# Performance work log

Hardware: AMD Instinct MI355X
Metric: run time of the kernel (lower is better)

## Reference

```python
import jax, jax.numpy as jnp
import numpy as np

WD = 8        # window_dim
E = 32        # embedding_dim
D = E * WD * WD   # attention_dim = 2048
NH = 8        # num_heads (SwinTransformer default)
B, H, W = 16, 64, 64
NW = (H // WD) * (W // WD)  # 64 windows
FF = 4 * D


def _partition(x):
    # 'b (vp vw) (hp hw) e -> b (vw hw) (vp hp e)', vp=hp=WD (patches are the OUTER factor)
    b, h, w, e = x.shape
    vw, hw = h // WD, w // WD
    x = x.reshape(b, WD, vw, WD, hw, e)
    x = x.transpose(0, 2, 4, 1, 3, 5)           # b vw hw vp hp e
    return x.reshape(b, vw * hw, WD * WD * e)   # [B, NW, D]


def _layer_norm(x, g, b, eps=1e-5):
    m = jnp.mean(x, axis=-1, keepdims=True)
    v = jnp.mean(jnp.square(x - m), axis=-1, keepdims=True)
    return (x - m) * jax.lax.rsqrt(v + eps) * g + b


def setup_inputs() -> dict:
    key = jax.random.key(0)
    ks = jax.random.split(key, 8)
    s = 0.02  # weight scale to keep activations sane at D=2048
    return {
        'embeddings': jax.random.normal(ks[0], (B, H, W, E), jnp.float32),
        'ln1_g': jnp.ones((D,), jnp.float32),
        'ln1_b': jnp.zeros((D,), jnp.float32),
        'wq': jax.random.normal(ks[1], (D, D), jnp.float32) * s,
        'bq': jnp.zeros((D,), jnp.float32),
        'wk': jax.random.normal(ks[2], (D, D), jnp.float32) * s,
        'bk': jnp.zeros((D,), jnp.float32),
        'wv': jax.random.normal(ks[3], (D, D), jnp.float32) * s,
        'bv': jnp.zeros((D,), jnp.float32),
        'pos_bias': jnp.zeros((NW, NW), jnp.float32),  # source discards the randn Parameter; bias is zeros
        'ln2_g': jnp.ones((D,), jnp.float32),
        'ln2_b': jnp.zeros((D,), jnp.float32),
        'w1': jax.random.normal(ks[4], (D, FF), jnp.float32) * s,
        'b1': jnp.zeros((FF,), jnp.float32),
        'w2': jax.random.normal(ks[5], (FF, D), jnp.float32) * s,
        'b2': jnp.zeros((D,), jnp.float32),
    }


def reference(embeddings, ln1_g, ln1_b, wq, bq, wk, bk, wv, bv, pos_bias,
              ln2_g, ln2_b, w1, b1, w2, b2):
    windows = _partition(embeddings)                       # [B, NW, D]
    x = _layer_norm(windows, ln1_g, ln1_b)
    hd = D // NH

    def heads(y):  # [B, NW, D] -> [B, NH, NW, hd]  (heads are outer factor)
        return y.reshape(B, NW, NH, hd).transpose(0, 2, 1, 3)

    q = heads(x @ wq + bq)
    k = heads(x @ wk + bk)
    v = heads(x @ wv + bv)

    logits = jnp.einsum('bhnd,bhmd->bhnm', q, k) / jnp.sqrt(jnp.float32(D)) + pos_bias
    # diagonal self-attention mask (eye) applied with -inf, then softmax over keys
    diag = jnp.eye(NW, dtype=bool)
    logits = jnp.where(diag, -jnp.inf, logits)
    attn = jax.nn.softmax(logits, axis=-1)                 # [B, NH, NW, NW]

    sa = jnp.einsum('bhnm,bhmd->bhnd', attn, v)            # [B, NH, NW, hd]
    sa = sa.transpose(0, 2, 1, 3).reshape(B, NW, D)

    attn_out = windows + sa
    y = _layer_norm(attn_out, ln2_g, ln2_b)
    y = jax.nn.gelu(y @ w1 + b1, approximate=False)
    y = y @ w2 + b2
    return attn_out + y                                    # [B, NW, D]
```

## Files before the change

kernel.cpp:

```cpp
#include <hip/hip_runtime.h>
#include <math.h>

#define ROWS 1024
#define DIM  2048
#define FFDIM 8192
#define NHEAD 8
#define HD 256
#define NWIN 64

typedef __attribute__((ext_vector_type(8))) short short8;
typedef __attribute__((ext_vector_type(4))) float f32x4;
typedef unsigned int uint32;

#define MFMA16(a, b, c) __builtin_amdgcn_mfma_f32_16x16x32_bf16((a), (b), (c), 0, 0, 0)

__device__ __forceinline__ uint32 pack_hi2(float a, float b) {
  return (__float_as_uint(a) >> 16) | (__float_as_uint(b) & 0xFFFF0000u);
}
__device__ __forceinline__ float trunc_hi(float a) {
  return __uint_as_float(__float_as_uint(a) & 0xFFFF0000u);
}
#define SWZ(r) (((r) >> 1) & 3)

template <int MI, int EPI>
__device__ __forceinline__ void gemm_body(
    const float* __restrict__ A, const float* __restrict__ W,
    const float* __restrict__ bias, const float* __restrict__ R,
    float* __restrict__ C, int N, int K, int kbeg, int kend, int m0, int n0,
    short* Ah, short* Al, short* Bh, short* Bl) {
  const int t = threadIdx.x;
  const int lane = t & 63;
  const int wid = t >> 6;
  const int wr = wid >> 1, wc = wid & 1;
  const int l15 = lane & 15, l4 = lane >> 4;

  const int arow = t >> 3, akq = t & 7;
  const int bn = t & 127, bkc = t >> 7;

  f32x4 acc[MI][4];
#pragma unroll
  for (int i = 0; i < MI; ++i)
#pragma unroll
    for (int j = 0; j < 4; ++j) {
      f32x4 z = {0.f, 0.f, 0.f, 0.f};
      acc[i][j] = z;
    }

  int aoff[MI], boff[4];
#pragma unroll
  for (int mi = 0; mi < MI; ++mi) {
    int m = wr * MI * 16 + mi * 16 + l15;
    aoff[mi] = m * 64 + ((l4 ^ SWZ(m)) << 4);
  }
#pragma unroll
  for (int ni = 0; ni < 4; ++ni) {
    int n = wc * 64 + ni * 16 + l15;
    boff[ni] = n * 64 + ((l4 ^ SWZ(n)) << 4);
  }

  const float* aptr = A + (size_t)(m0 + arow) * K + akq * 4;
  const float* bptr = W + (size_t)bkc * 16 * N + n0 + bn;

  float4 av[MI];
  float bv[16];
#pragma unroll
  for (int it = 0; it < MI; ++it)
    av[it] = *(const float4*)(aptr + (size_t)(it * 32) * K + kbeg);
#pragma unroll
  for (int i = 0; i < 16; ++i)
    bv[i] = bptr[(size_t)(kbeg + i) * N];

  for (int k0 = kbeg; k0 < kend; k0 += 32) {
    __syncthreads();

#pragma unroll
    for (int it = 0; it < MI; ++it) {
      const int row = arow + it * 32;
      const int off = row * 64 + (((akq >> 1) ^ SWZ(row)) << 4) + (akq & 1) * 8;
      const float x = av[it].x, y = av[it].y, z = av[it].z, w = av[it].w;
      uint32 h0 = pack_hi2(x, y), h1 = pack_hi2(z, w);
      uint32 L0 = pack_hi2(x - trunc_hi(x), y - trunc_hi(y));
      uint32 L1 = pack_hi2(z - trunc_hi(z), w - trunc_hi(w));
      *(uint2*)((char*)Ah + off) = make_uint2(h0, h1);
      *(uint2*)((char*)Al + off) = make_uint2(L0, L1);
    }
    {
      uint32 hh[8], ll[8];
#pragma unroll
      for (int j = 0; j < 8; ++j) {
        const float a = bv[2 * j], b = bv[2 * j + 1];
        hh[j] = pack_hi2(a, b);
        ll[j] = pack_hi2(a - trunc_hi(a), b - trunc_hi(b));
      }
      const int s0 = bn * 64 + (((bkc * 2) ^ SWZ(bn)) << 4);
      const int s1 = bn * 64 + (((bkc * 2 + 1) ^ SWZ(bn)) << 4);
      *(uint4*)((char*)Bh + s0) = make_uint4(hh[0], hh[1], hh[2], hh[3]);
      *(uint4*)((char*)Bh + s1) = make_uint4(hh[4], hh[5], hh[6], hh[7]);
      *(uint4*)((char*)Bl + s0) = make_uint4(ll[0], ll[1], ll[2], ll[3]);
      *(uint4*)((char*)Bl + s1) = make_uint4(ll[4], ll[5], ll[6], ll[7]);
    }
    __syncthreads();

    if (k0 + 32 < kend) {
#pragma unroll
      for (int it = 0; it < MI; ++it)
        av[it] = *(const float4*)(aptr + (size_t)(it * 32) * K + (k0 + 32));
#pragma unroll
      for (int i = 0; i < 16; ++i)
        bv[i] = bptr[(size_t)(k0 + 32 + i) * N];
    }

    short8 ah[MI], al[MI], bh[4], bl[4];
#pragma unroll
    for (int mi = 0; mi < MI; ++mi) {
      ah[mi] = *(const short8*)((const char*)Ah + aoff[mi]);
      al[mi] = *(const short8*)((const char*)Al + aoff[mi]);
    }
#pragma unroll
    for (int ni = 0; ni < 4; ++ni) {
      bh[ni] = *(const short8*)((const char*)Bh + boff[ni]);
      bl[ni] = *(const short8*)((const char*)Bl + boff[ni]);
    }
#pragma unroll
    for (int mi = 0; mi < MI; ++mi)
#pragma unroll
      for (int ni = 0; ni < 4; ++ni) {
        acc[mi][ni] = MFMA16(ah[mi], bh[ni], acc[mi][ni]);
        acc[mi][ni] = MFMA16(ah[mi], bl[ni], acc[mi][ni]);
        acc[mi][ni] = MFMA16(al[mi], bh[ni], acc[mi][ni]);
      }
  }

#pragma unroll
  for (int ni = 0; ni < 4; ++ni) {
    const int n = n0 + wc * 64 + ni * 16 + l15;
    const float bb = (EPI == 3) ? 0.f : bias[n];
#pragma unroll
    for (int mi = 0; mi < MI; ++mi) {
      const int mbase = m0 + wr * MI * 16 + mi * 16 + l4 * 4;
#pragma unroll
      for (int r = 0; r < 4; ++r) {
        float x = acc[mi][ni][r] + bb;
        const size_t idx = (size_t)(mbase + r) * N + n;
        if (EPI == 1) {
          x = 0.5f * x * (1.0f + erff(x * 0.70710678118654752f));
        } else if (EPI == 2) {
          x += R[idx];
        }
        C[idx] = x;
      }
    }
  }
}

template <int MI, int EPI>
__global__ __launch_bounds__(256, 2)
void gemm_k(const float* __restrict__ A, const float* __restrict__ W,
            const float* __restrict__ bias, const float* __restrict__ R,
            float* __restrict__ C, int N, int K, int ksplit) {
  __shared__ short Ah[MI * 1024], Al[MI * 1024], Bh[4096], Bl[4096];
  const int kbeg = blockIdx.z * ksplit;
  float* Ceff = C + (size_t)blockIdx.z * ROWS * N;
  gemm_body<MI, EPI>(A, W, bias, R, Ceff, N, K, kbeg, kbeg + ksplit,
                     blockIdx.y * MI * 32, blockIdx.x * 128, Ah, Al, Bh, Bl);
}

__global__ __launch_bounds__(256, 2)
void qkv_k(const float* __restrict__ A,
           const float* __restrict__ wq, const float* __restrict__ bq,
           const float* __restrict__ wk, const float* __restrict__ bk,
           const float* __restrict__ wv, const float* __restrict__ bv,
           float* __restrict__ q) {
  __shared__ short Ah[4096], Al[4096], Bh[4096], Bl[4096];
  const int nb = blockIdx.x;
  const int mat = nb >> 4;
  const float* W = (mat == 0) ? wq : (mat == 1) ? wk : wv;
  const float* B = (mat == 0) ? bq : (mat == 1) ? bk : bv;
  float* out = q + (size_t)mat * ROWS * DIM;
  gemm_body<4, 0>(A, W, B, nullptr, out, DIM, DIM, 0, DIM, blockIdx.y * 128,
                  (nb & 15) * 128, Ah, Al, Bh, Bl);
}

__global__ __launch_bounds__(256)
void reduce4_kernel(const float* __restrict__ p, const float* __restrict__ bias,
                    const float* __restrict__ R, float* __restrict__ out) {
  const int idx = blockIdx.x * 256 + threadIdx.x;
  const size_t PS = (size_t)ROWS * DIM / 4;
  const float4* p4 = (const float4*)p;
  float4 s0 = p4[idx], s1 = p4[idx + PS], s2 = p4[idx + 2 * PS], s3 = p4[idx + 3 * PS];
  const int n = (idx & (DIM / 4 - 1)) * 4;
  float4 bi = *(const float4*)&bias[n];
  float4 rr = ((const float4*)R)[idx];
  float4 o;
  o.x = s0.x + s1.x + s2.x + s3.x + bi.x + rr.x;
  o.y = s0.y + s1.y + s2.y + s3.y + bi.y + rr.y;
  o.z = s0.z + s1.z + s2.z + s3.z + bi.z + rr.z;
  o.w = s0.w + s1.w + s2.w + s3.w + bi.w + rr.w;
  ((float4*)out)[idx] = o;
}

__device__ inline void block_stats(float s, float ss, float& mean, float& rstd) {
#pragma unroll
  for (int off = 32; off; off >>= 1) {
    s  += __shfl_xor(s,  off);
    ss += __shfl_xor(ss, off);
  }
  __shared__ float red[8];
  const int t = threadIdx.x;
  const int w = t >> 6;
  if ((t & 63) == 0) { red[w] = s; red[4 | w] = ss; }
  __syncthreads();
  s  = red[0] + red[1] + red[2] + red[3];
  ss = red[4] + red[5] + red[6] + red[7];
  mean = s * (1.0f / DIM);
  float var = ss * (1.0f / DIM) - mean * mean;
  rstd = 1.0f / sqrtf(var + 1e-5f);
}

__global__ __launch_bounds__(256)
void partition_ln1_kernel(const float* __restrict__ emb,
                          const float* __restrict__ g, const float* __restrict__ be,
                          float* __restrict__ windows, float* __restrict__ xln) {
  const int row = blockIdx.x;
  const int b = row >> 6, n = row & 63;
  const int vw = n >> 3, hw = n & 7;
  const int t = threadIdx.x;
  const int d0 = t * 4, d1 = d0 + 1024;

  const int vp0 = d0 >> 8, hp0 = (d0 >> 5) & 7, e0 = d0 & 31;
  const int vp1 = d1 >> 8, hp1 = (d1 >> 5) & 7, e1 = d1 & 31;
  float4 v0 = *(const float4*)&emb[(size_t)(((b*64 + vp0*8 + vw)*64) + hp0*8 + hw)*32 + e0];
  float4 v1 = *(const float4*)&emb[(size_t)(((b*64 + vp1*8 + vw)*64) + hp1*8 + hw)*32 + e1];

  float s  = v0.x+v0.y+v0.z+v0.w + v1.x+v1.y+v1.z+v1.w;
  float ss = v0.x*v0.x+v0.y*v0.y+v0.z*v0.z+v0.w*v0.w
           + v1.x*v1.x+v1.y*v1.y+v1.z*v1.z+v1.w*v1.w;
  float mean, rstd;
  block_stats(s, ss, mean, rstd);

  float* wrow = windows + (size_t)row * DIM;
  *(float4*)&wrow[d0] = v0;
  *(float4*)&wrow[d1] = v1;

  float4 g0 = *(const float4*)&g[d0],  g1 = *(const float4*)&g[d1];
  float4 b0 = *(const float4*)&be[d0], b1 = *(const float4*)&be[d1];
  float4 o0, o1;
  o0.x = (v0.x-mean)*rstd*g0.x + b0.x; o0.y = (v0.y-mean)*rstd*g0.y + b0.y;
  o0.z = (v0.z-mean)*rstd*g0.z + b0.z; o0.w = (v0.w-mean)*rstd*g0.w + b0.w;
  o1.x = (v1.x-mean)*rstd*g1.x + b1.x; o1.y = (v1.y-mean)*rstd*g1.y + b1.y;
  o1.z = (v1.z-mean)*rstd*g1.z + b1.z; o1.w = (v1.w-mean)*rstd*g1.w + b1.w;
  float* xrow = xln + (size_t)row * DIM;
  *(float4*)&xrow[d0] = o0;
  *(float4*)&xrow[d1] = o1;
}

__global__ __launch_bounds__(256)
void ln_kernel(const float* __restrict__ in, const float* __restrict__ g,
               const float* __restrict__ be, float* __restrict__ out) {
  const int row = blockIdx.x;
  const int t = threadIdx.x;
  const float* x = in + (size_t)row * DIM;
  const int d0 = t * 4, d1 = d0 + 1024;
  float4 v0 = *(const float4*)&x[d0];
  float4 v1 = *(const float4*)&x[d1];
  float s  = v0.x+v0.y+v0.z+v0.w + v1.x+v1.y+v1.z+v1.w;
  float ss = v0.x*v0.x+v0.y*v0.y+v0.z*v0.z+v0.w*v0.w
           + v1.x*v1.x+v1.y*v1.y+v1.z*v1.z+v1.w*v1.w;
  float mean, rstd;
  block_stats(s, ss, mean, rstd);
  float4 g0 = *(const float4*)&g[d0],  g1 = *(const float4*)&g[d1];
  float4 b0 = *(const float4*)&be[d0], b1 = *(const float4*)&be[d1];
  float4 o0, o1;
  o0.x = (v0.x-mean)*rstd*g0.x + b0.x; o0.y = (v0.y-mean)*rstd*g0.y + b0.y;
  o0.z = (v0.z-mean)*rstd*g0.z + b0.z; o0.w = (v0.w-mean)*rstd*g0.w + b0.w;
  o1.x = (v1.x-mean)*rstd*g1.x + b1.x; o1.y = (v1.y-mean)*rstd*g1.y + b1.y;
  o1.z = (v1.z-mean)*rstd*g1.z + b1.z; o1.w = (v1.w-mean)*rstd*g1.w + b1.w;
  float* orow = out + (size_t)row * DIM;
  *(float4*)&orow[d0] = o0;
  *(float4*)&orow[d1] = o1;
}

__global__ __launch_bounds__(256)
void attn_kernel(const float* __restrict__ Q, const float* __restrict__ K,
                 const float* __restrict__ V, const float* __restrict__ pb,
                 const float* __restrict__ windows, float* __restrict__ attn_out) {
  __shared__ float kv[NWIN][HD];
  __shared__ float qs[32][HD + 4];
  __shared__ float att[32][NWIN + 1];
  const int blk = blockIdx.x;
  const int bh = blk >> 1, half = blk & 1;
  const int b = bh >> 3, h = bh & 7;
  const int qbase = half * 32;
  const int t = threadIdx.x;
  const size_t base = (size_t)b * 64 * DIM + (size_t)h * HD;

#pragma unroll
  for (int j = 0; j < 16; ++j) {
    int idx = t + j * 256;
    int m = idx >> 6, dg = idx & 63;
    *(float4*)&kv[m][dg * 4] = *(const float4*)&K[base + (size_t)m * DIM + dg * 4];
  }
#pragma unroll
  for (int j = 0; j < 8; ++j) {
    int idx = t + j * 256;
    int m = idx >> 6, dg = idx & 63;
    *(float4*)&qs[m][dg * 4] = *(const float4*)&Q[base + (size_t)(qbase + m) * DIM + dg * 4];
  }
  __syncthreads();

  {
    const int n = t & 31;
    const int m0 = (t >> 5) * 8;
    float acc[8];
#pragma unroll
    for (int j = 0; j < 8; ++j) acc[j] = 0.f;
    for (int dg = 0; dg < 64; ++dg) {
      float4 qv = *(const float4*)&qs[n][dg * 4];
#pragma unroll
      for (int j = 0; j < 8; ++j) {
        const float* kr = &kv[m0 + j][dg * 4];
        acc[j] += qv.x * kr[0] + qv.y * kr[1] + qv.z * kr[2] + qv.w * kr[3];
      }
    }
    const float scale = 0.022097086912079608f;
#pragma unroll
    for (int j = 0; j < 8; ++j) {
      const int m = m0 + j;
      float l = acc[j] * scale + pb[(qbase + n) * 64 + m];
      if (m == qbase + n) l = -INFINITY;
      att[n][m] = l;
    }
  }
  __syncthreads();

#pragma unroll
  for (int j = 0; j < 16; ++j) {
    int idx = t + j * 256;
    int m = idx >> 6, dg = idx & 63;
    *(float4*)&kv[m][dg * 4] = *(const float4*)&V[base + (size_t)m * DIM + dg * 4];
  }
  if (t < 32) {
    float mx = -INFINITY;
#pragma unroll
    for (int m = 0; m < 64; ++m) mx = fmaxf(mx, att[t][m]);
    float sum = 0.f;
#pragma unroll
    for (int m = 0; m < 64; ++m) {
      float e = expf(att[t][m] - mx);
      att[t][m] = e;
      sum += e;
    }
    float inv = 1.0f / sum;
#pragma unroll
    for (int m = 0; m < 64; ++m) att[t][m] *= inv;
  }
  __syncthreads();

  {
    const int dg = t & 63, nh = t >> 6;
#pragma unroll
    for (int i = 0; i < 8; ++i) {
      const int nn = nh * 8 + i;
      float4 s = make_float4(0.f, 0.f, 0.f, 0.f);
      for (int m = 0; m < 64; ++m) {
        const float a = att[nn][m];
        const float* vr = &kv[m][dg * 4];
        s.x = fmaf(a, vr[0], s.x); s.y = fmaf(a, vr[1], s.y);
        s.z = fmaf(a, vr[2], s.z); s.w = fmaf(a, vr[3], s.w);
      }
      const size_t o = base + (size_t)(qbase + nn) * DIM + dg * 4;
      float4 w4 = *(const float4*)&windows[o];
      s.x += w4.x; s.y += w4.y; s.z += w4.z; s.w += w4.w;
      *(float4*)&attn_out[o] = s;
    }
  }
}

extern "C" void kernel_launch(void* const* d_in, const int* in_sizes, int n_in,
                              void* d_out, int out_size, void* d_ws, size_t ws_size,
                              hipStream_t stream) {
  const float* emb  = (const float*)d_in[0];
  const float* ln1g = (const float*)d_in[1];
  const float* ln1b = (const float*)d_in[2];
  const float* wq   = (const float*)d_in[3];
  const float* bq   = (const float*)d_in[4];
  const float* wk   = (const float*)d_in[5];
  const float* bk   = (const float*)d_in[6];
  const float* wv   = (const float*)d_in[7];
  const float* bv   = (const float*)d_in[8];
  const float* pb   = (const float*)d_in[9];
  const float* ln2g = (const float*)d_in[10];
  const float* ln2b = (const float*)d_in[11];
  const float* w1   = (const float*)d_in[12];
  const float* b1   = (const float*)d_in[13];
  const float* w2   = (const float*)d_in[14];
  const float* b2   = (const float*)d_in[15];
  float* out = (float*)d_out;

  float* ws = (float*)d_ws;
  const size_t OFF = (size_t)ROWS * DIM;
  float* windows  = ws;
  float* xln      = ws + OFF;
  float* q        = ws + 2 * OFF;
  float* attn_out = ws + 5 * OFF;
  float* ffh      = ws + 6 * OFF;
  float* partial  = ws;

  partition_ln1_kernel<<<ROWS, 256, 0, stream>>>(emb, ln1g, ln1b, windows, xln);

  qkv_k<<<dim3(48, 8), 256, 0, stream>>>(xln, wq, bq, wk, bk, wv, bv, q);

  attn_kernel<<<16 * NHEAD * 2, 256, 0, stream>>>(q, q + OFF, q + 2 * OFF, pb,
                                                  windows, attn_out);

  ln_kernel<<<ROWS, 256, 0, stream>>>(attn_out, ln2g, ln2b, xln);

  gemm_k<4, 1><<<dim3(FFDIM / 128, ROWS / 128, 1), 256, 0, stream>>>(
      xln, w1, b1, nullptr, ffh, FFDIM, DIM, DIM);
  gemm_k<4, 3><<<dim3(DIM / 128, ROWS / 128, 4), 256, 0, stream>>>(
      ffh, w2, nullptr, nullptr, partial, DIM, FFDIM, FFDIM / 4);
  reduce4_kernel<<<(ROWS * DIM / 4) / 256, 256, 0, stream>>>(partial, b2, attn_out, out);
}
```

Measured before the change: 551.5 us.

## Switch GEMMs from split-bf16 3xMFMA to single bf16 with pre-transposed weights

Drops the hi/lo bf16 split emulation of fp32 (three MFMAs per tile) for a single bf16 MFMA. Weights are converted and transposed to bf16 on each call by a new conversion kernel, and activations (LN outputs, QKV, FFN hidden) are stored as bf16 to halve traffic. The attention kernel is reworked to read bf16 Q/K/V and uses a register-blocked QK and AV loop. This cuts MFMA work and memory bandwidth but lowers accuracy and adds per-call weight conversion passes.

```diff
diff --git a/kernel.cpp b/kernel.cpp
--- a/kernel.cpp
+++ b/kernel.cpp
@@ -7,35 +7,63 @@
 #define NHEAD 8
 #define HD 256
 #define NWIN 64
+#define MB (1u << 20)
 
 typedef __attribute__((ext_vector_type(8))) short short8;
 typedef __attribute__((ext_vector_type(4))) float f32x4;
 typedef unsigned int uint32;
+typedef unsigned short ushort_t;
 
 #define MFMA16(a, b, c) __builtin_amdgcn_mfma_f32_16x16x32_bf16((a), (b), (c), 0, 0, 0)
-
-__device__ __forceinline__ uint32 pack_hi2(float a, float b) {
-  return (__float_as_uint(a) >> 16) | (__float_as_uint(b) & 0xFFFF0000u);
-}
-__device__ __forceinline__ float trunc_hi(float a) {
-  return __uint_as_float(__float_as_uint(a) & 0xFFFF0000u);
-}
 #define SWZ(r) (((r) >> 1) & 3)
+
+__device__ __forceinline__ ushort_t rne(float x) {
+  uint32 u = __float_as_uint(x);
+  return (ushort_t)((u + 0x7FFFu + ((u >> 16) & 1u)) >> 16);
+}
+__device__ __forceinline__ float bf2f(ushort_t h) {
+  return __uint_as_float(((uint32)h) << 16);
+}
+
+__global__ __launch_bounds__(256)
+void wconvT_kernel(const float* __restrict__ s0, const float* __restrict__ s1,
+                   const float* __restrict__ s2, ushort_t* __restrict__ d,
+                   int R, int C) {
+  const float* src = (blockIdx.z == 0) ? s0 : (blockIdx.z == 1) ? s1 : s2;
+  ushort_t* dst = d + (size_t)blockIdx.z * R * C;
+  __shared__ float tl[64][65];
+  const int r0 = blockIdx.y * 64, c0 = blockIdx.x * 64;
+  const int tr = threadIdx.x >> 4, tc = threadIdx.x & 15;
+#pragma unroll
+  for (int i = 0; i < 4; ++i) {
+    const int r = tr + i * 16;
+    float4 v = *(const float4*)&src[(size_t)(r0 + r) * C + c0 + tc * 4];
+    tl[r][tc * 4 + 0] = v.x; tl[r][tc * 4 + 1] = v.y;
+    tl[r][tc * 4 + 2] = v.z; tl[r][tc * 4 + 3] = v.w;
+  }
+  __syncthreads();
+#pragma unroll
+  for (int i = 0; i < 4; ++i) {
+    const int c = tr + i * 16;
+    ushort4 o;
+    o.x = rne(tl[tc * 4 + 0][c]); o.y = rne(tl[tc * 4 + 1][c]);
+    o.z = rne(tl[tc * 4 + 2][c]); o.w = rne(tl[tc * 4 + 3][c]);
+    *(ushort4*)&dst[(size_t)(c0 + c) * R + r0 + tc * 4] = o;
+  }
+}
 
 template <int MI, int EPI>
 __device__ __forceinline__ void gemm_body(
-    const float* __restrict__ A, const float* __restrict__ W,
-    const float* __restrict__ bias, const float* __restrict__ R,
-    float* __restrict__ C, int N, int K, int kbeg, int kend, int m0, int n0,
-    short* Ah, short* Al, short* Bh, short* Bl) {
+    const ushort_t* __restrict__ A, const ushort_t* __restrict__ Bt,
+    const float* __restrict__ bias, float* __restrict__ Cf,
+    ushort_t* __restrict__ C16, int N, int K, int kbeg, int kend,
+    int m0, int n0, short* As, short* Bs) {
   const int t = threadIdx.x;
   const int lane = t & 63;
   const int wid = t >> 6;
   const int wr = wid >> 1, wc = wid & 1;
   const int l15 = lane & 15, l4 = lane >> 4;
-
-  const int arow = t >> 3, akq = t & 7;
-  const int bn = t & 127, bkc = t >> 7;
+  constexpr int ACH = MI / 2;
 
   f32x4 acc[MI][4];
 #pragma unroll
@@ -58,77 +86,58 @@
     boff[ni] = n * 64 + ((l4 ^ SWZ(n)) << 4);
   }
 
-  const float* aptr = A + (size_t)(m0 + arow) * K + akq * 4;
-  const float* bptr = W + (size_t)bkc * 16 * N + n0 + bn;
-
-  float4 av[MI];
-  float bv[16];
-#pragma unroll
-  for (int it = 0; it < MI; ++it)
-    av[it] = *(const float4*)(aptr + (size_t)(it * 32) * K + kbeg);
-#pragma unroll
-  for (int i = 0; i < 16; ++i)
-    bv[i] = bptr[(size_t)(kbeg + i) * N];
+  const int srow = t >> 2, sq = t & 3;
+  const ushort_t* aptr = A + (size_t)(m0 + srow) * K + sq * 8;
+  const ushort_t* bptr = Bt + (size_t)(n0 + srow) * K + sq * 8;
+  int awoff[ACH], bwoff[2];
+#pragma unroll
+  for (int j = 0; j < ACH; ++j) {
+    const int row = srow + j * 64;
+    awoff[j] = row * 64 + ((sq ^ SWZ(row)) << 4);
+  }
+#pragma unroll
+  for (int j = 0; j < 2; ++j) {
+    const int row = srow + j * 64;
+    bwoff[j] = row * 64 + ((sq ^ SWZ(row)) << 4);
+  }
+
+  uint4 pa[ACH], pb[2];
+#pragma unroll
+  for (int j = 0; j < ACH; ++j)
+    pa[j] = *(const uint4*)(aptr + (size_t)(j * 64) * K + kbeg);
+#pragma unroll
+  for (int j = 0; j < 2; ++j)
+    pb[j] = *(const uint4*)(bptr + (size_t)(j * 64) * K + kbeg);
 
   for (int k0 = kbeg; k0 < kend; k0 += 32) {
     __syncthreads();
-
-#pragma unroll
-    for (int it = 0; it < MI; ++it) {
-      const int row = arow + it * 32;
-      const int off = row * 64 + (((akq >> 1) ^ SWZ(row)) << 4) + (akq & 1) * 8;
-      const float x = av[it].x, y = av[it].y, z = av[it].z, w = av[it].w;
-      uint32 h0 = pack_hi2(x, y), h1 = pack_hi2(z, w);
-      uint32 L0 = pack_hi2(x - trunc_hi(x), y - trunc_hi(y));
-      uint32 L1 = pack_hi2(z - trunc_hi(z), w - trunc_hi(w));
-      *(uint2*)((char*)Ah + off) = make_uint2(h0, h1);
-      *(uint2*)((char*)Al + off) = make_uint2(L0, L1);
-    }
-    {
-      uint32 hh[8], ll[8];
-#pragma unroll
-      for (int j = 0; j < 8; ++j) {
-        const float a = bv[2 * j], b = bv[2 * j + 1];
-        hh[j] = pack_hi2(a, b);
-        ll[j] = pack_hi2(a - trunc_hi(a), b - trunc_hi(b));
-      }
-      const int s0 = bn * 64 + (((bkc * 2) ^ SWZ(bn)) << 4);
-      const int s1 = bn * 64 + (((bkc * 2 + 1) ^ SWZ(bn)) << 4);
-      *(uint4*)((char*)Bh + s0) = make_uint4(hh[0], hh[1], hh[2], hh[3]);
-      *(uint4*)((char*)Bh + s1) = make_uint4(hh[4], hh[5], hh[6], hh[7]);
-      *(uint4*)((char*)Bl + s0) = make_uint4(ll[0], ll[1], ll[2], ll[3]);
-      *(uint4*)((char*)Bl + s1) = make_uint4(ll[4], ll[5], ll[6], ll[7]);
-    }
+#pragma unroll
+    for (int j = 0; j < ACH; ++j) *(uint4*)((char*)As + awoff[j]) = pa[j];
+#pragma unroll
+    for (int j = 0; j < 2; ++j)   *(uint4*)((char*)Bs + bwoff[j]) = pb[j];
     __syncthreads();
 
     if (k0 + 32 < kend) {
 #pragma unroll
-      for (int it = 0; it < MI; ++it)
-        av[it] = *(const float4*)(aptr + (size_t)(it * 32) * K + (k0 + 32));
-#pragma unroll
-      for (int i = 0; i < 16; ++i)
-        bv[i] = bptr[(size_t)(k0 + 32 + i) * N];
-    }
-
-    short8 ah[MI], al[MI], bh[4], bl[4];
-#pragma unroll
-    for (int mi = 0; mi < MI; ++mi) {
-      ah[mi] = *(const short8*)((const char*)Ah + aoff[mi]);
-      al[mi] = *(const short8*)((const char*)Al + aoff[mi]);
-    }
-#pragma unroll
-    for (int ni = 0; ni < 4; ++ni) {
-      bh[ni] = *(const short8*)((const char*)Bh + boff[ni]);
-      bl[ni] = *(const short8*)((const char*)Bl + boff[ni]);
-    }
+      for (int j = 0; j < ACH; ++j)
+        pa[j] = *(const uint4*)(aptr + (size_t)(j * 64) * K + (k0 + 32));
+#pragma unroll
+      for (int j = 0; j < 2; ++j)
+        pb[j] = *(const uint4*)(bptr + (size_t)(j * 64) * K + (k0 + 32));
+    }
+
+    short8 a[MI], b4[4];
 #pragma unroll
     for (int mi = 0; mi < MI; ++mi)
-#pragma unroll
-      for (int ni = 0; ni < 4; ++ni) {
-        acc[mi][ni] = MFMA16(ah[mi], bh[ni], acc[mi][ni]);
-        acc[mi][ni] = MFMA16(ah[mi], bl[ni], acc[mi][ni]);
-        acc[mi][ni] = MFMA16(al[mi], bh[ni], acc[mi][ni]);
-      }
+      a[mi] = *(const short8*)((const char*)As + aoff[mi]);
+#pragma unroll
+    for (int ni = 0; ni < 4; ++ni)
+      b4[ni] = *(const short8*)((const char*)Bs + boff[ni]);
+#pragma unroll
+    for (int mi = 0; mi < MI; ++mi)
+#pragma unroll
+      for (int ni = 0; ni < 4; ++ni)
+        acc[mi][ni] = MFMA16(a[mi], b4[ni], acc[mi][ni]);
   }
 
 #pragma unroll
@@ -142,12 +151,14 @@
       for (int r = 0; r < 4; ++r) {
         float x = acc[mi][ni][r] + bb;
         const size_t idx = (size_t)(mbase + r) * N + n;
-        if (EPI == 1) {
+        if (EPI == 0) {
+          C16[idx] = rne(x);
+        } else if (EPI == 1) {
           x = 0.5f * x * (1.0f + erff(x * 0.70710678118654752f));
-        } else if (EPI == 2) {
-          x += R[idx];
+          C16[idx] = rne(x);
+        } else {
+          Cf[idx] = x;
         }
-        C[idx] = x;
       }
     }
   }
@@ -155,30 +166,30 @@
 
 template <int MI, int EPI>
 __global__ __launch_bounds__(256, 2)
-void gemm_k(const float* __restrict__ A, const float* __restrict__ W,
-            const float* __restrict__ bias, const float* __restrict__ R,
-            float* __restrict__ C, int N, int K, int ksplit) {
-  __shared__ short Ah[MI * 1024], Al[MI * 1024], Bh[4096], Bl[4096];
+void gemm_k(const ushort_t* __restrict__ A, const ushort_t* __restrict__ Bt,
+            const float* __restrict__ bias, float* __restrict__ Cf,
+            ushort_t* __restrict__ C16, int N, int K, int ksplit) {
+  __shared__ __align__(16) short As[MI * 1024];
+  __shared__ __align__(16) short Bs[4096];
   const int kbeg = blockIdx.z * ksplit;
-  float* Ceff = C + (size_t)blockIdx.z * ROWS * N;
-  gemm_body<MI, EPI>(A, W, bias, R, Ceff, N, K, kbeg, kbeg + ksplit,
-                     blockIdx.y * MI * 32, blockIdx.x * 128, Ah, Al, Bh, Bl);
-}
-
-__global__ __launch_bounds__(256, 2)
-void qkv_k(const float* __restrict__ A,
-           const float* __restrict__ wq, const float* __restrict__ bq,
-           const float* __restrict__ wk, const float* __restrict__ bk,
-           const float* __restrict__ wv, const float* __restrict__ bv,
-           float* __restrict__ q) {
-  __shared__ short Ah[4096], Al[4096], Bh[4096], Bl[4096];
+  float* Cfe = (EPI == 3) ? Cf + (size_t)blockIdx.z * ROWS * N : Cf;
+  gemm_body<MI, EPI>(A, Bt, bias, Cfe, C16, N, K, kbeg, kbeg + ksplit,
+                     blockIdx.y * MI * 32, blockIdx.x * 128, As, Bs);
+}
+
+__global__ __launch_bounds__(256, 3)
+void qkv_k(const ushort_t* __restrict__ A, const ushort_t* __restrict__ qkvT,
+           const float* __restrict__ bq, const float* __restrict__ bk,
+           const float* __restrict__ bv, ushort_t* __restrict__ outq) {
+  __shared__ __align__(16) short As[2048];
+  __shared__ __align__(16) short Bs[4096];
   const int nb = blockIdx.x;
   const int mat = nb >> 4;
-  const float* W = (mat == 0) ? wq : (mat == 1) ? wk : wv;
+  const ushort_t* W = qkvT + (size_t)mat * DIM * DIM;
   const float* B = (mat == 0) ? bq : (mat == 1) ? bk : bv;
-  float* out = q + (size_t)mat * ROWS * DIM;
-  gemm_body<4, 0>(A, W, B, nullptr, out, DIM, DIM, 0, DIM, blockIdx.y * 128,
-                  (nb & 15) * 128, Ah, Al, Bh, Bl);
+  ushort_t* out = outq + (size_t)mat * ROWS * DIM;
+  gemm_body<2, 0>(A, W, B, nullptr, out, DIM, DIM, 0, DIM,
+                  blockIdx.y * 64, (nb & 15) * 128, As, Bs);
 }
 
 __global__ __launch_bounds__(256)
@@ -220,7 +231,7 @@
 __global__ __launch_bounds__(256)
 void partition_ln1_kernel(const float* __restrict__ emb,
                           const float* __restrict__ g, const float* __restrict__ be,
-                          float* __restrict__ windows, float* __restrict__ xln) {
+                          float* __restrict__ windows, ushort_t* __restrict__ xbf) {
   const int row = blockIdx.x;
   const int b = row >> 6, n = row & 63;
   const int vw = n >> 3, hw = n & 7;
@@ -244,19 +255,18 @@
 
   float4 g0 = *(const float4*)&g[d0],  g1 = *(const float4*)&g[d1];
   float4 b0 = *(const float4*)&be[d0], b1 = *(const float4*)&be[d1];
-  float4 o0, o1;
-  o0.x = (v0.x-mean)*rstd*g0.x + b0.x; o0.y = (v0.y-mean)*rstd*g0.y + b0.y;
-  o0.z = (v0.z-mean)*rstd*g0.z + b0.z; o0.w = (v0.w-mean)*rstd*g0.w + b0.w;
-  o1.x = (v1.x-mean)*rstd*g1.x + b1.x; o1.y = (v1.y-mean)*rstd*g1.y + b1.y;
-  o1.z = (v1.z-mean)*rstd*g1.z + b1.z; o1.w = (v1.w-mean)*rstd*g1.w + b1.w;
-  float* xrow = xln + (size_t)row * DIM;
-  *(float4*)&xrow[d0] = o0;
-  *(float4*)&xrow[d1] = o1;
+  ushort4 o0, o1;
+  o0.x = rne((v0.x-mean)*rstd*g0.x + b0.x); o0.y = rne((v0.y-mean)*rstd*g0.y + b0.y);
+  o0.z = rne((v0.z-mean)*rstd*g0.z + b0.z); o0.w = rne((v0.w-mean)*rstd*g0.w + b0.w);
+  o1.x = rne((v1.x-mean)*rstd*g1.x + b1.x); o1.y = rne((v1.y-mean)*rstd*g1.y + b1.y);
+  o1.z = rne((v1.z-mean)*rstd*g1.z + b1.z); o1.w = rne((v1.w-mean)*rstd*g1.w + b1.w);
+  *(ushort4*)&xbf[(size_t)row * DIM + d0] = o0;
+  *(ushort4*)&xbf[(size_t)row * DIM + d1] = o1;
 }
 
 __global__ __launch_bounds__(256)
 void ln_kernel(const float* __restrict__ in, const float* __restrict__ g,
-               const float* __restrict__ be, float* __restrict__ out) {
+               const float* __restrict__ be, ushort_t* __restrict__ out) {
   const int row = blockIdx.x;
   const int t = threadIdx.x;
   const float* x = in + (size_t)row * DIM;
@@ -270,22 +280,21 @@
   block_stats(s, ss, mean, rstd);
   float4 g0 = *(const float4*)&g[d0],  g1 = *(const float4*)&g[d1];
   float4 b0 = *(const float4*)&be[d0], b1 = *(const float4*)&be[d1];
-  float4 o0, o1;
-  o0.x = (v0.x-mean)*rstd*g0.x + b0.x; o0.y = (v0.y-mean)*rstd*g0.y + b0.y;
-  o0.z = (v0.z-mean)*rstd*g0.z + b0.z; o0.w = (v0.w-mean)*rstd*g0.w + b0.w;
-  o1.x = (v1.x-mean)*rstd*g1.x + b1.x; o1.y = (v1.y-mean)*rstd*g1.y + b1.y;
-  o1.z = (v1.z-mean)*rstd*g1.z + b1.z; o1.w = (v1.w-mean)*rstd*g1.w + b1.w;
-  float* orow = out + (size_t)row * DIM;
-  *(float4*)&orow[d0] = o0;
-  *(float4*)&orow[d1] = o1;
+  ushort4 o0, o1;
+  o0.x = rne((v0.x-mean)*rstd*g0.x + b0.x); o0.y = rne((v0.y-mean)*rstd*g0.y + b0.y);
+  o0.z = rne((v0.z-mean)*rstd*g0.z + b0.z); o0.w = rne((v0.w-mean)*rstd*g0.w + b0.w);
+  o1.x = rne((v1.x-mean)*rstd*g1.x + b1.x); o1.y = rne((v1.y-mean)*rstd*g1.y + b1.y);
+  o1.z = rne((v1.z-mean)*rstd*g1.z + b1.z); o1.w = rne((v1.w-mean)*rstd*g1.w + b1.w);
+  *(ushort4*)&out[(size_t)row * DIM + d0] = o0;
+  *(ushort4*)&out[(size_t)row * DIM + d1] = o1;
 }
 
 __global__ __launch_bounds__(256)
-void attn_kernel(const float* __restrict__ Q, const float* __restrict__ K,
-                 const float* __restrict__ V, const float* __restrict__ pb,
+void attn_kernel(const ushort_t* __restrict__ Q, const ushort_t* __restrict__ K,
+                 const ushort_t* __restrict__ V, const float* __restrict__ pb,
                  const float* __restrict__ windows, float* __restrict__ attn_out) {
-  __shared__ float kv[NWIN][HD];
-  __shared__ float qs[32][HD + 4];
+  __shared__ __align__(16) float kv[NWIN][264];
+  __shared__ __align__(16) float qs[32][268];
   __shared__ float att[32][NWIN + 1];
   const int blk = blockIdx.x;
   const int bh = blk >> 1, half = blk & 1;
@@ -295,49 +304,72 @@
   const size_t base = (size_t)b * 64 * DIM + (size_t)h * HD;
 
 #pragma unroll
-  for (int j = 0; j < 16; ++j) {
-    int idx = t + j * 256;
-    int m = idx >> 6, dg = idx & 63;
-    *(float4*)&kv[m][dg * 4] = *(const float4*)&K[base + (size_t)m * DIM + dg * 4];
-  }
-#pragma unroll
   for (int j = 0; j < 8; ++j) {
     int idx = t + j * 256;
-    int m = idx >> 6, dg = idx & 63;
-    *(float4*)&qs[m][dg * 4] = *(const float4*)&Q[base + (size_t)(qbase + m) * DIM + dg * 4];
+    int m = idx >> 5, c8 = idx & 31;
+    uint4 raw = *(const uint4*)&K[base + (size_t)m * DIM + c8 * 8];
+    float4 f0 = {bf2f((ushort_t)(raw.x & 0xffff)), bf2f((ushort_t)(raw.x >> 16)),
+                 bf2f((ushort_t)(raw.y & 0xffff)), bf2f((ushort_t)(raw.y >> 16))};
+    float4 f1 = {bf2f((ushort_t)(raw.z & 0xffff)), bf2f((ushort_t)(raw.z >> 16)),
+                 bf2f((ushort_t)(raw.w & 0xffff)), bf2f((ushort_t)(raw.w >> 16))};
+    *(float4*)&kv[m][c8 * 8] = f0;
+    *(float4*)&kv[m][c8 * 8 + 4] = f1;
+  }
+#pragma unroll
+  for (int j = 0; j < 4; ++j) {
+    int idx = t + j * 256;
+    int m = idx >> 5, c8 = idx & 31;
+    uint4 raw = *(const uint4*)&Q[base + (size_t)(qbase + m) * DIM + c8 * 8];
+    float4 f0 = {bf2f((ushort_t)(raw.x & 0xffff)), bf2f((ushort_t)(raw.x >> 16)),
+                 bf2f((ushort_t)(raw.y & 0xffff)), bf2f((ushort_t)(raw.y >> 16))};
+    float4 f1 = {bf2f((ushort_t)(raw.z & 0xffff)), bf2f((ushort_t)(raw.z >> 16)),
+                 bf2f((ushort_t)(raw.w & 0xffff)), bf2f((ushort_t)(raw.w >> 16))};
+    *(float4*)&qs[m][c8 * 8] = f0;
+    *(float4*)&qs[m][c8 * 8 + 4] = f1;
   }
   __syncthreads();
 
   {
-    const int n = t & 31;
-    const int m0 = (t >> 5) * 8;
-    float acc[8];
-#pragma unroll
-    for (int j = 0; j < 8; ++j) acc[j] = 0.f;
+    const int rp = t & 15;
+    const int kg = t >> 4;
+    float acc[2][4] = {};
     for (int dg = 0; dg < 64; ++dg) {
-      float4 qv = *(const float4*)&qs[n][dg * 4];
-#pragma unroll
-      for (int j = 0; j < 8; ++j) {
-        const float* kr = &kv[m0 + j][dg * 4];
-        acc[j] += qv.x * kr[0] + qv.y * kr[1] + qv.z * kr[2] + qv.w * kr[3];
+      float4 q0 = *(const float4*)&qs[rp][dg * 4];
+      float4 q1 = *(const float4*)&qs[rp + 16][dg * 4];
+#pragma unroll
+      for (int j = 0; j < 4; ++j) {
+        float4 kr = *(const float4*)&kv[4 * kg + j][dg * 4];
+        acc[0][j] += q0.x * kr.x + q0.y * kr.y + q0.z * kr.z + q0.w * kr.w;
+        acc[1][j] += q1.x * kr.x + q1.y * kr.y + q1.z * kr.z + q1.w * kr.w;
       }
     }
     const float scale = 0.022097086912079608f;
 #pragma unroll
-    for (int j = 0; j < 8; ++j) {
-      const int m = m0 + j;
-      float l = acc[j] * scale + pb[(qbase + n) * 64 + m];
-      if (m == qbase + n) l = -INFINITY;
-      att[n][m] = l;
+    for (int i = 0; i < 2; ++i) {
+      const int rl = rp + i * 16;
+      const int gr = qbase + rl;
+#pragma unroll
+      for (int j = 0; j < 4; ++j) {
+        const int m = 4 * kg + j;
+        float l = acc[i][j] * scale + pb[gr * 64 + m];
+        if (m == gr) l = -INFINITY;
+        att[rl][m] = l;
+      }
     }
   }
   __syncthreads();
 
 #pragma unroll
-  for (int j = 0; j < 16; ++j) {
+  for (int j = 0; j < 8; ++j) {
     int idx = t + j * 256;
-    int m = idx >> 6, dg = idx & 63;
-    *(float4*)&kv[m][dg * 4] = *(const float4*)&V[base + (size_t)m * DIM + dg * 4];
+    int m = idx >> 5, c8 = idx & 31;
+    uint4 raw = *(const uint4*)&V[base + (size_t)m * DIM + c8 * 8];
+    float4 f0 = {bf2f((ushort_t)(raw.x & 0xffff)), bf2f((ushort_t)(raw.x >> 16)),
+                 bf2f((ushort_t)(raw.y & 0xffff)), bf2f((ushort_t)(raw.y >> 16))};
+    float4 f1 = {bf2f((ushort_t)(raw.z & 0xffff)), bf2f((ushort_t)(raw.z >> 16)),
+                 bf2f((ushort_t)(raw.w & 0xffff)), bf2f((ushort_t)(raw.w >> 16))};
+    *(float4*)&kv[m][c8 * 8] = f0;
+    *(float4*)&kv[m][c8 * 8 + 4] = f1;
   }
   if (t < 32) {
     float mx = -INFINITY;
@@ -357,21 +389,28 @@
   __syncthreads();
 
   {
-    const int dg = t & 63, nh = t >> 6;
+    const int dg = t & 63, rg = t >> 6;
+    float4 s[8];
+#pragma unroll
+    for (int i = 0; i < 8; ++i) s[i] = make_float4(0.f, 0.f, 0.f, 0.f);
+    for (int m = 0; m < 64; ++m) {
+      float4 vr = *(const float4*)&kv[m][dg * 4];
+#pragma unroll
+      for (int i = 0; i < 8; ++i) {
+        const float a = att[rg * 8 + i][m];
+        s[i].x = fmaf(a, vr.x, s[i].x); s[i].y = fmaf(a, vr.y, s[i].y);
+        s[i].z = fmaf(a, vr.z, s[i].z); s[i].w = fmaf(a, vr.w, s[i].w);
+      }
+    }
 #pragma unroll
     for (int i = 0; i < 8; ++i) {
-      const int nn = nh * 8 + i;
-      float4 s = make_float4(0.f, 0.f, 0.f, 0.f);
-      for (int m = 0; m < 64; ++m) {
-        const float a = att[nn][m];
-        const float* vr = &kv[m][dg * 4];
-        s.x = fmaf(a, vr[0], s.x); s.y = fmaf(a, vr[1], s.y);
-        s.z = fmaf(a, vr[2], s.z); s.w = fmaf(a, vr[3], s.w);
-      }
-      const size_t o = base + (size_t)(qbase + nn) * DIM + dg * 4;
+      const int row = qbase + rg * 8 + i;
+      const size_t o = base + (size_t)row * DIM + dg * 4;
       float4 w4 = *(const float4*)&windows[o];
-      s.x += w4.x; s.y += w4.y; s.z += w4.z; s.w += w4.w;
-      *(float4*)&attn_out[o] = s;
+      float4 r;
+      r.x = s[i].x + w4.x; r.y = s[i].y + w4.y;
+      r.z = s[i].z + w4.z; r.w = s[i].w + w4.w;
+      *(float4*)&attn_out[o] = r;
     }
   }
 }
@@ -397,27 +436,35 @@
   const float* b2   = (const float*)d_in[15];
   float* out = (float*)d_out;
 
-  float* ws = (float*)d_ws;
+  char* W8 = (char*)d_ws;
+  float*    windows  = (float*)(W8 + (size_t)0 * MB);
+  ushort_t* xbf      = (ushort_t*)(W8 + (size_t)8 * MB);
+  ushort_t* w1T      = (ushort_t*)(W8 + (size_t)12 * MB);
+  ushort_t* qb       = (ushort_t*)(W8 + (size_t)44 * MB);
+  float*    attn_out = (float*)(W8 + (size_t)56 * MB);
+  ushort_t* qkvT     = (ushort_t*)(W8 + (size_t)64 * MB);
+  ushort_t* w2T      = (ushort_t*)(W8 + (size_t)64 * MB);
+  ushort_t* ffh      = (ushort_t*)(W8 + (size_t)96 * MB);
+  float*    partial  = (float*)(W8 + (size_t)0 * MB);
   const size_t OFF = (size_t)ROWS * DIM;
-  float* windows  = ws;
-  float* xln      = ws + OFF;
-  float* q        = ws + 2 * OFF;
-  float* attn_out = ws + 5 * OFF;
-  float* ffh      = ws + 6 * OFF;
-  float* partial  = ws;
-
-  partition_ln1_kernel<<<ROWS, 256, 0, stream>>>(emb, ln1g, ln1b, windows, xln);
-
-  qkv_k<<<dim3(48, 8), 256, 0, stream>>>(xln, wq, bq, wk, bk, wv, bv, q);
-
-  attn_kernel<<<16 * NHEAD * 2, 256, 0, stream>>>(q, q + OFF, q + 2 * OFF, pb,
+
+  wconvT_kernel<<<dim3(32, 32, 3), 256, 0, stream>>>(wq, wk, wv, qkvT, DIM, DIM);
+  wconvT_kernel<<<dim3(128, 32, 1), 256, 0, stream>>>(w1, w1, w1, w1T, DIM, FFDIM);
+
+  partition_ln1_kernel<<<ROWS, 256, 0, stream>>>(emb, ln1g, ln1b, windows, xbf);
+
+  qkv_k<<<dim3(48, 16), 256, 0, stream>>>(xbf, qkvT, bq, bk, bv, qb);
+
+  attn_kernel<<<16 * NHEAD * 2, 256, 0, stream>>>(qb, qb + OFF, qb + 2 * OFF, pb,
                                                   windows, attn_out);
 
-  ln_kernel<<<ROWS, 256, 0, stream>>>(attn_out, ln2g, ln2b, xln);
-
-  gemm_k<4, 1><<<dim3(FFDIM / 128, ROWS / 128, 1), 256, 0, stream>>>(
-      xln, w1, b1, nullptr, ffh, FFDIM, DIM, DIM);
-  gemm_k<4, 3><<<dim3(DIM / 128, ROWS / 128, 4), 256, 0, stream>>>(
-      ffh, w2, nullptr, nullptr, partial, DIM, FFDIM, FFDIM / 4);
+  wconvT_kernel<<<dim3(32, 128, 1), 256, 0, stream>>>(w2, w2, w2, w2T, FFDIM, DIM);
+
+  ln_kernel<<<ROWS, 256, 0, stream>>>(attn_out, ln2g, ln2b, xbf);
+
+  gemm_k<4, 1><<<dim3(64, 8, 1), 256, 0, stream>>>(
+      xbf, w1T, b1, nullptr, ffh, FFDIM, DIM, DIM);
+  gemm_k<4, 3><<<dim3(16, 8, 4), 256, 0, stream>>>(
+      ffh, w2T, nullptr, partial, nullptr, DIM, FFDIM, FFDIM / 4);
   reduce4_kernel<<<(ROWS * DIM / 4) / 256, 256, 0, stream>>>(partial, b2, attn_out, out);
 }
```

New measurement: 655.7 us. 18.9% more time.
